# Kernel tuning notes

Measured on AMD Instinct MI355X. Metric: run time of the kernel, lower is better.

## Reference

```python
import jax, jax.numpy as jnp
import numpy as np

K, STRIDE, PAD = 3, 1, 1


def _unfold(x, k=K, stride=STRIDE, pad=PAD):
    # x: [B, C, H, W] -> patches [B, C*k*k, L] (im2col, torch nn.Unfold layout:
    # channel index = c*k*k + ki*k + kj)
    p = jax.lax.conv_general_dilated_patches(
        x, filter_shape=(k, k), window_strides=(stride, stride),
        padding=((pad, pad), (pad, pad)))  # [B, C*k*k, Ho, Wo]
    B = x.shape[0]
    return p.reshape(B, p.shape[1], -1)


def reference(x, weight, dweight, bias):
    B, C, H, W = x.shape
    O = weight.shape[0]
    cols = _unfold(x)                                   # [B, C*k*k, L]
    # scalar gate per spatial position: dweight . sigmoid(cols)
    gate = jnp.einsum('f,bfl->bl', dweight.reshape(-1), jax.nn.sigmoid(cols))
    gated = cols * gate[:, None, :]                     # [B, C*k*k, L]
    out = jnp.einsum('of,bfl->bol', weight.reshape(O, -1), gated)  # [B, O, L]
    out = out + bias[None, :, None]
    Ho, Wo = (H // 2, W // 2) if STRIDE == 2 else (H, W)
    return out.reshape(B, O, Ho, Wo)


def setup_inputs() -> dict:
    key = jax.random.key(0)
    k1, k2, k3, k4 = jax.random.split(key, 4)
    B, C, O, H, W = 8, 32, 32, 256, 256
    fan_out = O * K * K
    std = float(np.sqrt(2.0 / fan_out))
    return {
        'x': jax.random.normal(k1, (B, C, H, W), dtype=jnp.float32),
        'weight': jax.random.normal(k2, (O, C, K, K), dtype=jnp.float32) * std,
        'dweight': jax.random.normal(k3, (1, C, K, K), dtype=jnp.float32) * std,
        'bias': jax.random.normal(k4, (O,), dtype=jnp.float32),
    }
```

## Files before the change

kernel.cpp:

```cpp
#include <hip/hip_runtime.h>


typedef _Float16 half8 __attribute__((ext_vector_type(8)));
typedef _Float16 half2 __attribute__((ext_vector_type(2)));
typedef float f32x16 __attribute__((ext_vector_type(16)));

#define BATCH 8
#define CIN 32
#define COUT 32
#define HH 256
#define WW 256
#define TW 32
#define TH 8
#define HTW 34
#define HTH 10
#define CSTR 40
#define NCHUNK 18
#define NLDSA 12
#define NREGA (NCHUNK - NLDSA)
#define NPOS (HTH*HTW)

__global__ __launch_bounds__(256) void prep_pack(const float* __restrict__ w,
                                                 const float* __restrict__ dw,
                                                 _Float16* __restrict__ Apack,
                                                 half2* __restrict__ dwf2) {
  int t = blockIdx.x * 256 + threadIdx.x;
  if (t < 9216) {
    int q = t >> 9, lane = (t >> 3) & 63, j = t & 7;
    int tap = q >> 1, h = q & 1;
    int o = lane & 31, lh = lane >> 5;
    int c = h * 16 + lh * 8 + j;
    Apack[t] = (_Float16)w[o * 288 + c * 9 + tap];
  } else if (t < 9216 + 144) {
    int i = t - 9216;
    int cp = i / 9, tap = i - cp * 9;
    half2 d;
    d.x = (_Float16)dw[(2 * cp) * 9 + tap];
    d.y = (_Float16)dw[(2 * cp + 1) * 9 + tap];
    dwf2[i] = d;
  }
}

__global__ __launch_bounds__(512, 6) void dynconv(
    const float* __restrict__ x, const _Float16* __restrict__ Apack,
    const half2* __restrict__ dwf2, const float* __restrict__ bias,
    float* __restrict__ out) {
  __shared__ __align__(16) _Float16 lvA[NLDSA * 512];
  __shared__ __align__(16) _Float16 lv[NPOS * CSTR];
  __shared__ _Float16 gpart[9 * NPOS];

  const int bid0 = blockIdx.x;
  const int bb = bid0 & 7, idx = bid0 >> 3;
  const int xt = idx & 7, yt = idx >> 3;
  const int x0 = xt * TW, y0 = yt * TH;
  const int tid = threadIdx.x;
  const int lane = tid & 63;

  half8 areg[NREGA];
#pragma unroll
  for (int r = 0; r < NREGA; ++r)
    areg[r] = *(const half8*)(Apack + (((NLDSA + r) * 64 + lane) << 3));

  half8 acopy0 = *(const half8*)(Apack + (tid << 3));
  half8 acopy1;
  if (tid < NLDSA * 64 - 512)
    acopy1 = *(const half8*)(Apack + ((512 + tid) << 3));

  const bool owner = tid < NPOS;
  float v[CIN];
  if (owner) {
    const int yy = tid / HTW, xx = tid - (tid / HTW) * HTW;
    const int gy = y0 + yy - 1, gx = x0 + xx - 1;
    const int voff = (gy << 8) + gx;
    if ((unsigned)gy < 256u && (unsigned)gx < 256u) {
#pragma unroll
      for (int c = 0; c < CIN; ++c)
        v[c] = x[(((size_t)(bb * CIN + c)) << 16) + voff];
    } else {
#pragma unroll
      for (int c = 0; c < CIN; ++c) v[c] = 0.f;
    }
  }

  *(half8*)(lvA + (tid << 3)) = acopy0;
  if (tid < NLDSA * 64 - 512)
    *(half8*)(lvA + ((512 + tid) << 3)) = acopy1;

  if (owner) {
    float p[9];
#pragma unroll
    for (int tap = 0; tap < 9; ++tap) p[tap] = 0.f;
    _Float16 hv[CIN];
#pragma unroll
    for (int cp = 0; cp < CIN / 2; ++cp) {
      const float v0 = v[2 * cp], v1 = v[2 * cp + 1];
      const float s0 = __builtin_amdgcn_rcpf(1.f + __expf(-v0));
      const float s1 = __builtin_amdgcn_rcpf(1.f + __expf(-v1));
      half2 s2;
      s2.x = (_Float16)s0;
      s2.y = (_Float16)s1;
      hv[2 * cp] = (_Float16)v0;
      hv[2 * cp + 1] = (_Float16)v1;
#pragma unroll
      for (int tap = 0; tap < 9; ++tap) {
        const half2 d2 = dwf2[cp * 9 + tap];
#if __has_builtin(__builtin_amdgcn_fdot2)
        p[tap] = __builtin_amdgcn_fdot2(s2, d2, p[tap], false);
#else
        p[tap] += (float)s2.x * (float)d2.x + (float)s2.y * (float)d2.y;
#endif
      }
    }
#pragma unroll
    for (int u = 0; u < 4; ++u)
      *(half8*)(lv + tid * CSTR + u * 8) = *(const half8*)(hv + u * 8);
#pragma unroll
    for (int tap = 0; tap < 9; ++tap)
      gpart[tap * NPOS + tid] = (_Float16)p[tap];
  }
  __syncthreads();

  const int w8 = tid >> 6;
  const int ln = lane & 31, lh = lane >> 5;

  float gate = 0.f;
#pragma unroll
  for (int ki = 0; ki < 3; ++ki)
#pragma unroll
    for (int kj = 0; kj < 3; ++kj)
      gate += (float)gpart[(ki * 3 + kj) * NPOS + (w8 + ki) * HTW + ln + kj];

  f32x16 acc;
#pragma unroll
  for (int i = 0; i < 16; ++i) acc[i] = 0.f;

#pragma unroll
  for (int q = 0; q < NCHUNK; ++q) {
    const int tap = q >> 1, h = q & 1;
    const int ki = tap / 3, kj = tap - ki * 3;
    const half8 a = (q < NLDSA)
                        ? *(const half8*)(lvA + ((q * 64 + lane) << 3))
                        : areg[q - NLDSA];
    const int off = ((w8 + ki) * HTW + ln + kj) * CSTR + h * 16 + lh * 8;
    const half8 bv = *(const half8*)(lv + off);
    acc = __builtin_amdgcn_mfma_f32_32x32x16_f16(a, bv, acc, 0, 0, 0);
  }

  const int voff_out = ((y0 + w8) << 8) + x0 + ln;
#pragma unroll
  for (int reg = 0; reg < 16; ++reg) {
    const int o = (reg & 3) + 8 * (reg >> 2) + 4 * lh;
    out[(((size_t)(bb * COUT + o)) << 16) + voff_out] = acc[reg] * gate + bias[o];
  }
}

extern "C" void kernel_launch(void* const* d_in, const int* in_sizes, int n_in,
                              void* d_out, int out_size, void* d_ws, size_t ws_size,
                              hipStream_t stream) {
  const float* x    = (const float*)d_in[0];
  const float* wgt  = (const float*)d_in[1];
  const float* dw   = (const float*)d_in[2];
  const float* bias = (const float*)d_in[3];
  float* out = (float*)d_out;

  _Float16* Apack = (_Float16*)d_ws;
  half2* dwf2     = (half2*)((char*)d_ws + 18432);

  prep_pack<<<(9216 + 144 + 255) / 256, 256, 0, stream>>>(wgt, dw, Apack, dwf2);
  dynconv<<<BATCH * (HH / TH) * (WW / TW), 512, 0, stream>>>(x, Apack, dwf2, bias, out);
}
```

Before: 133.4 us.

## Process four x-tiles per block with double-buffered LDS and prefetched input

Each block now walks four consecutive 32-wide tiles along x instead of one, double-buffering the fp16 patch and gate-partial LDS arrays. While the sigmoid and gate partials for the current tile are computed, the next tile's input is loaded, which overlaps global loads with compute. This also amortizes the weight staging over more work. In exchange there are four times fewer blocks (512 total), lower occupancy (launch bound 4 instead of 6), more LDS per block, and adjacent tiles re-read their halo columns.

```diff
diff --git a/kernel.cpp b/kernel.cpp
--- a/kernel.cpp
+++ b/kernel.cpp
@@ -8,17 +8,16 @@
 #define BATCH 8
 #define CIN 32
 #define COUT 32
-#define HH 256
-#define WW 256
 #define TW 32
 #define TH 8
 #define HTW 34
 #define HTH 10
 #define CSTR 40
 #define NCHUNK 18
-#define NLDSA 12
+#define NLDSA 14
 #define NREGA (NCHUNK - NLDSA)
 #define NPOS (HTH*HTW)
+#define NT 4
 
 __global__ __launch_bounds__(256) void prep_pack(const float* __restrict__ w,
                                                  const float* __restrict__ dw,
@@ -41,18 +40,18 @@
   }
 }
 
-__global__ __launch_bounds__(512, 6) void dynconv(
+__global__ __launch_bounds__(512, 4) void dynconv(
     const float* __restrict__ x, const _Float16* __restrict__ Apack,
     const half2* __restrict__ dwf2, const float* __restrict__ bias,
     float* __restrict__ out) {
   __shared__ __align__(16) _Float16 lvA[NLDSA * 512];
-  __shared__ __align__(16) _Float16 lv[NPOS * CSTR];
-  __shared__ _Float16 gpart[9 * NPOS];
+  __shared__ __align__(16) _Float16 lv[2][NPOS * CSTR];
+  __shared__ _Float16 gpart[2][9 * NPOS];
 
   const int bid0 = blockIdx.x;
   const int bb = bid0 & 7, idx = bid0 >> 3;
-  const int xt = idx & 7, yt = idx >> 3;
-  const int x0 = xt * TW, y0 = yt * TH;
+  const int xh = idx & 1, yt = idx >> 1;
+  const int x0b = xh * (NT * TW), y0 = yt * TH;
   const int tid = threadIdx.x;
   const int lane = tid & 63;
 
@@ -67,15 +66,17 @@
     acopy1 = *(const half8*)(Apack + ((512 + tid) << 3));
 
   const bool owner = tid < NPOS;
+  const int yy = tid / HTW, xx = tid - (tid / HTW) * HTW;
+  const int gy = y0 + yy - 1;
+  const bool rowok = (unsigned)gy < 256u;
+
   float v[CIN];
   if (owner) {
-    const int yy = tid / HTW, xx = tid - (tid / HTW) * HTW;
-    const int gy = y0 + yy - 1, gx = x0 + xx - 1;
-    const int voff = (gy << 8) + gx;
-    if ((unsigned)gy < 256u && (unsigned)gx < 256u) {
+    const int gx = x0b + xx - 1;
+    if (rowok && (unsigned)gx < 256u) {
 #pragma unroll
       for (int c = 0; c < CIN; ++c)
-        v[c] = x[(((size_t)(bb * CIN + c)) << 16) + voff];
+        v[c] = x[(((size_t)(bb * CIN + c)) << 16) + (gy << 8) + gx];
     } else {
 #pragma unroll
       for (int c = 0; c < CIN; ++c) v[c] = 0.f;
@@ -86,71 +87,90 @@
   if (tid < NLDSA * 64 - 512)
     *(half8*)(lvA + ((512 + tid) << 3)) = acopy1;
 
-  if (owner) {
-    float p[9];
-#pragma unroll
-    for (int tap = 0; tap < 9; ++tap) p[tap] = 0.f;
-    _Float16 hv[CIN];
-#pragma unroll
-    for (int cp = 0; cp < CIN / 2; ++cp) {
-      const float v0 = v[2 * cp], v1 = v[2 * cp + 1];
-      const float s0 = __builtin_amdgcn_rcpf(1.f + __expf(-v0));
-      const float s1 = __builtin_amdgcn_rcpf(1.f + __expf(-v1));
-      half2 s2;
-      s2.x = (_Float16)s0;
-      s2.y = (_Float16)s1;
-      hv[2 * cp] = (_Float16)v0;
-      hv[2 * cp + 1] = (_Float16)v1;
-#pragma unroll
-      for (int tap = 0; tap < 9; ++tap) {
-        const half2 d2 = dwf2[cp * 9 + tap];
-#if __has_builtin(__builtin_amdgcn_fdot2)
-        p[tap] = __builtin_amdgcn_fdot2(s2, d2, p[tap], false);
-#else
-        p[tap] += (float)s2.x * (float)d2.x + (float)s2.y * (float)d2.y;
-#endif
-      }
-    }
-#pragma unroll
-    for (int u = 0; u < 4; ++u)
-      *(half8*)(lv + tid * CSTR + u * 8) = *(const half8*)(hv + u * 8);
-#pragma unroll
-    for (int tap = 0; tap < 9; ++tap)
-      gpart[tap * NPOS + tid] = (_Float16)p[tap];
-  }
-  __syncthreads();
-
   const int w8 = tid >> 6;
   const int ln = lane & 31, lh = lane >> 5;
 
-  float gate = 0.f;
 #pragma unroll
-  for (int ki = 0; ki < 3; ++ki)
+  for (int t = 0; t < NT; ++t) {
+    const int buf = t & 1;
+
+    float p[9];
+    _Float16 hv[CIN];
+    if (owner) {
 #pragma unroll
-    for (int kj = 0; kj < 3; ++kj)
-      gate += (float)gpart[(ki * 3 + kj) * NPOS + (w8 + ki) * HTW + ln + kj];
+      for (int tap = 0; tap < 9; ++tap) p[tap] = 0.f;
+#pragma unroll
+      for (int cp = 0; cp < CIN / 2; ++cp) {
+        const float v0 = v[2 * cp], v1 = v[2 * cp + 1];
+        const float s0 = __builtin_amdgcn_rcpf(1.f + __expf(-v0));
+        const float s1 = __builtin_amdgcn_rcpf(1.f + __expf(-v1));
+        half2 s2;
+        s2.x = (_Float16)s0;
+        s2.y = (_Float16)s1;
+        hv[2 * cp] = (_Float16)v0;
+        hv[2 * cp + 1] = (_Float16)v1;
+#pragma unroll
+        for (int tap = 0; tap < 9; ++tap) {
+          const half2 d2 = dwf2[cp * 9 + tap];
+#if __has_builtin(__builtin_amdgcn_fdot2)
+          p[tap] = __builtin_amdgcn_fdot2(s2, d2, p[tap], false);
+#else
+          p[tap] += (float)s2.x * (float)d2.x + (float)s2.y * (float)d2.y;
+#endif
+        }
+      }
+      if (t + 1 < NT) {
+        const int gx = x0b + (t + 1) * TW + xx - 1;
+        if (rowok && (unsigned)gx < 256u) {
+#pragma unroll
+          for (int c = 0; c < CIN; ++c)
+            v[c] = x[(((size_t)(bb * CIN + c)) << 16) + (gy << 8) + gx];
+        } else {
+#pragma unroll
+          for (int c = 0; c < CIN; ++c) v[c] = 0.f;
+        }
+      }
+#pragma unroll
+      for (int u = 0; u < 4; ++u)
+        *(half8*)(&lv[buf][tid * CSTR + u * 8]) = *(const half8*)(hv + u * 8);
+#pragma unroll
+      for (int tap = 0; tap < 9; ++tap)
+        gpart[buf][tap * NPOS + tid] = (_Float16)p[tap];
+    }
 
-  f32x16 acc;
+    asm volatile("s_waitcnt lgkmcnt(0)" ::: "memory");
+    __builtin_amdgcn_s_barrier();
+    asm volatile("" ::: "memory");
+
+    float gate = 0.f;
 #pragma unroll
-  for (int i = 0; i < 16; ++i) acc[i] = 0.f;
+    for (int ki = 0; ki < 3; ++ki)
+#pragma unroll
+      for (int kj = 0; kj < 3; ++kj)
+        gate += (float)gpart[buf][(ki * 3 + kj) * NPOS + (w8 + ki) * HTW + ln + kj];
+
+    f32x16 acc;
+#pragma unroll
+    for (int i = 0; i < 16; ++i) acc[i] = 0.f;
 
 #pragma unroll
-  for (int q = 0; q < NCHUNK; ++q) {
-    const int tap = q >> 1, h = q & 1;
-    const int ki = tap / 3, kj = tap - ki * 3;
-    const half8 a = (q < NLDSA)
-                        ? *(const half8*)(lvA + ((q * 64 + lane) << 3))
-                        : areg[q - NLDSA];
-    const int off = ((w8 + ki) * HTW + ln + kj) * CSTR + h * 16 + lh * 8;
-    const half8 bv = *(const half8*)(lv + off);
-    acc = __builtin_amdgcn_mfma_f32_32x32x16_f16(a, bv, acc, 0, 0, 0);
-  }
+    for (int q = 0; q < NCHUNK; ++q) {
+      const int tap = q >> 1, h = q & 1;
+      const int ki = tap / 3, kj = tap - ki * 3;
+      const half8 a = (q < NLDSA)
+                          ? *(const half8*)(lvA + ((q * 64 + lane) << 3))
+                          : areg[q - NLDSA];
+      const int off = ((w8 + ki) * HTW + ln + kj) * CSTR + h * 16 + lh * 8;
+      const half8 bv = *(const half8*)(&lv[buf][off]);
+      acc = __builtin_amdgcn_mfma_f32_32x32x16_f16(a, bv, acc, 0, 0, 0);
+    }
 
-  const int voff_out = ((y0 + w8) << 8) + x0 + ln;
+    const int voff_out = ((y0 + w8) << 8) + x0b + t * TW + ln;
 #pragma unroll
-  for (int reg = 0; reg < 16; ++reg) {
-    const int o = (reg & 3) + 8 * (reg >> 2) + 4 * lh;
-    out[(((size_t)(bb * COUT + o)) << 16) + voff_out] = acc[reg] * gate + bias[o];
+    for (int reg = 0; reg < 16; ++reg) {
+      const int o = (reg & 3) + 8 * (reg >> 2) + 4 * lh;
+      out[(((size_t)(bb * COUT + o)) << 16) + voff_out] = acc[reg] * gate + bias[o];
+    }
   }
 }
 
@@ -167,5 +187,5 @@
   half2* dwf2     = (half2*)((char*)d_ws + 18432);
 
   prep_pack<<<(9216 + 144 + 255) / 256, 256, 0, stream>>>(wgt, dw, Apack, dwf2);
-  dynconv<<<BATCH * (HH / TH) * (WW / TW), 512, 0, stream>>>(x, Apack, dwf2, bias, out);
+  dynconv<<<BATCH * 32 * 2, 512, 0, stream>>>(x, Apack, dwf2, bias, out);
 }
```

Result: slower. 157.3 us (+18.0%).
